# Kernel tuning notes

Hardware: AMD Instinct MI355X
Metric: run time of the kernel (lower is better)

The kernel has to match this reference:

```python
import jax, jax.numpy as jnp
import numpy as np

B, S, D, H = 4, 2048, 1024, 16
HD = D // H  # 64


def setup_inputs() -> dict:
    key = jax.random.key(0)
    ks = jax.random.split(key, 5)
    s = 1.0 / np.sqrt(D)
    return {
        "x": jax.random.normal(ks[0], (B, S, D), dtype=jnp.float32),
        "W_attn": jax.random.normal(ks[1], (D, 3 * D), dtype=jnp.float32) * s,
        "b_attn": jnp.zeros((3 * D,), dtype=jnp.float32),
        "W_proj": jax.random.normal(ks[2], (D, D), dtype=jnp.float32) * s,
        "b_proj": jnp.zeros((D,), dtype=jnp.float32),
    }


def reference(x, W_attn, b_attn, W_proj, b_proj):
    Bx, Sx, Dx = x.shape
    qkv = x @ W_attn + b_attn                      # [B,S,3D]
    q, k, v = jnp.split(qkv, 3, axis=-1)
    q = q.reshape(Bx, Sx, H, HD).transpose(0, 2, 1, 3)  # [B,H,S,hd]
    k = k.reshape(Bx, Sx, H, HD).transpose(0, 2, 1, 3)
    v = v.reshape(Bx, Sx, H, HD).transpose(0, 2, 1, 3)
    att = jnp.einsum('bhqd,bhkd->bhqk', q, k) * (HD ** -0.5)
    causal = jnp.tril(jnp.ones((Sx, Sx), dtype=bool))
    att = jnp.where(causal[None, None], att, -jnp.inf)
    att = jax.nn.softmax(att, axis=-1)
    y = jnp.einsum('bhqk,bhkd->bhqd', att, v)      # [B,H,S,hd]
    y = y.transpose(0, 2, 1, 3).reshape(Bx, Sx, Dx)
    return y @ W_proj + b_proj
```

## Files before the change

kernel.cpp:

```cpp
#include <hip/hip_runtime.h>
#include <hip/hip_bf16.h>
#include <math.h>


typedef __bf16 bf16;
typedef __bf16 bf16x8 __attribute__((ext_vector_type(8)));
typedef __bf16 bf16x4 __attribute__((ext_vector_type(4)));
typedef float f32x4 __attribute__((ext_vector_type(4)));

#define B_ 4
#define S_ 2048
#define D_ 1024
#define H_ 16
#define HD_ 64
#define QSCALE 0.1803368801f

#if __has_builtin(__builtin_amdgcn_exp2f)
#define EXP2F(x) __builtin_amdgcn_exp2f(x)
#else
#define EXP2F(x) exp2f(x)
#endif
#if __has_builtin(__builtin_amdgcn_rcpf)
#define RCPF(x) __builtin_amdgcn_rcpf(x)
#else
#define RCPF(x) (1.0f / (x))
#endif

#define GLOAD_LDS16(gptr, lptr)                                              \
    __builtin_amdgcn_global_load_lds(                                        \
        (const __attribute__((address_space(1))) void*)(uintptr_t)(gptr),    \
        (__attribute__((address_space(3))) void*)(uintptr_t)(lptr), 16, 0, 0)

__global__ void k_cvt(const float* __restrict__ in, bf16* __restrict__ out, int n) {
    int i = (blockIdx.x * 256 + threadIdx.x) * 4;
    if (i >= n) return;
    float4 v = *reinterpret_cast<const float4*>(in + i);
    bf16x4 o;
    o.x = (bf16)v.x; o.y = (bf16)v.y; o.z = (bf16)v.z; o.w = (bf16)v.w;
    *reinterpret_cast<bf16x4*>(out + i) = o;
}

__global__ void k_transpose_cvt(const float* __restrict__ W, bf16* __restrict__ WT,
                                int K, int N) {
    __shared__ float t[32][33];
    int n0 = blockIdx.x * 32, k0 = blockIdx.y * 32;
    int tx = threadIdx.x & 31, ty = threadIdx.x >> 5;
#pragma unroll
    for (int j = 0; j < 32; j += 8)
        t[ty + j][tx] = W[(size_t)(k0 + ty + j) * N + n0 + tx];
    __syncthreads();
#pragma unroll
    for (int j = 0; j < 32; j += 8)
        WT[(size_t)(n0 + ty + j) * K + k0 + tx] = (bf16)t[tx][ty + j];
}

template <int MODE>
__global__ __launch_bounds__(256) void k_gemm(
    const bf16* __restrict__ A, const bf16* __restrict__ BT,
    const float* __restrict__ bias,
    void* out0, void* out1, void* out2, int M, int N, int K) {
    __shared__ __align__(16) bf16 Asm[2][128][64];
    __shared__ __align__(16) bf16 Bsm[2][128][64];
    int mb = blockIdx.y * 128, nb = blockIdx.x * 128;
    int tid = threadIdx.x;
    int w = tid >> 6, lane = tid & 63, lo = lane & 15, qu = lane >> 4;
    int wm = (w >> 1) * 64, wn = (w & 1) * 64;
    int srow = lane >> 3, sch = lane & 7;
    int gch = (sch ^ srow) * 8;
    int r0 = w * 32;

    f32x4 zero = {0.f, 0.f, 0.f, 0.f};
    f32x4 acc[4][4];
#pragma unroll
    for (int i = 0; i < 4; i++)
#pragma unroll
        for (int j = 0; j < 4; j++) acc[i][j] = zero;

    const int nt = K >> 6;

    auto stage = [&](int t, int buf) {
        int kb = t * 64;
#pragma unroll
        for (int g = 0; g < 4; g++) {
            int row = r0 + g * 8;
            GLOAD_LDS16(A + (size_t)(mb + row + srow) * K + kb + gch,
                        &Asm[buf][row][0]);
            GLOAD_LDS16(BT + (size_t)(nb + row + srow) * K + kb + gch,
                        &Bsm[buf][row][0]);
        }
    };

    stage(0, 0);

    for (int t = 0; t < nt; t++) {
        int cur = t & 1;
        if (t + 1 < nt) {
            stage(t + 1, cur ^ 1);
            asm volatile("s_waitcnt vmcnt(8)" ::: "memory");
        } else {
            asm volatile("s_waitcnt vmcnt(0)" ::: "memory");
        }
        __builtin_amdgcn_s_barrier();
        asm volatile("" ::: "memory");
        bf16x8 af[4][2], bfr[4][2];
#pragma unroll
        for (int tt = 0; tt < 4; tt++)
#pragma unroll
            for (int ks = 0; ks < 2; ks++) {
                af[tt][ks] = *reinterpret_cast<const bf16x8*>(
                    &Asm[cur][wm + tt * 16 + lo][((ks * 4 + qu) ^ (lo & 7)) * 8]);
                bfr[tt][ks] = *reinterpret_cast<const bf16x8*>(
                    &Bsm[cur][wn + tt * 16 + lo][((ks * 4 + qu) ^ (lo & 7)) * 8]);
            }
        __builtin_amdgcn_s_setprio(1);
#pragma unroll
        for (int i = 0; i < 4; i++)
#pragma unroll
            for (int j = 0; j < 4; j++) {
                acc[i][j] = __builtin_amdgcn_mfma_f32_16x16x32_bf16(
                    af[i][0], bfr[j][0], acc[i][j], 0, 0, 0);
                acc[i][j] = __builtin_amdgcn_mfma_f32_16x16x32_bf16(
                    af[i][1], bfr[j][1], acc[i][j], 0, 0, 0);
            }
        __builtin_amdgcn_s_setprio(0);
        asm volatile("" ::: "memory");
        __builtin_amdgcn_s_barrier();
        asm volatile("" ::: "memory");
    }

#pragma unroll
    for (int i = 0; i < 4; i++) {
#pragma unroll
        for (int j = 0; j < 4; j++) {
            int col = nb + wn + j * 16 + lo;
            float bv = bias[col];
            float v4v[4];
#pragma unroll
            for (int r = 0; r < 4; r++) v4v[r] = acc[i][j][r] + bv;
            int row0 = mb + wm + i * 16 + qu * 4;
            if (MODE == 0) {
                int b = row0 >> 11, s0 = row0 & 2047;
                int which = col >> 10, rem = col & 1023;
                int h = rem >> 6, d = rem & 63;
                int bh = b * H_ + h;
                if (which == 2) {
                    bf16x4 pk;
#pragma unroll
                    for (int r = 0; r < 4; r++) pk[r] = (bf16)v4v[r];
                    *reinterpret_cast<bf16x4*>(
                        (bf16*)out2 + ((size_t)bh * HD_ + d) * S_ + s0) = pk;
                } else {
                    bf16* dst = which == 0 ? (bf16*)out0 : (bf16*)out1;
                    float sc = which == 0 ? QSCALE : 1.0f;
#pragma unroll
                    for (int r = 0; r < 4; r++)
                        dst[((size_t)bh * S_ + s0 + r) * HD_ + d] = (bf16)(v4v[r] * sc);
                }
            } else {
#pragma unroll
                for (int r = 0; r < 4; r++)
                    ((float*)out0)[(size_t)(row0 + r) * N + col] = v4v[r];
            }
        }
    }
}

__global__ __launch_bounds__(256) void k_attn(
    const bf16* __restrict__ Q, const bf16* __restrict__ K,
    const bf16* __restrict__ Vt, bf16* __restrict__ Y) {
    __shared__ __align__(16) bf16 Ks[2][64][64];
    __shared__ __align__(16) bf16 Vs[2][64][64];
    __shared__ __align__(16) bf16 Psm[4][32][68];
    int blk = blockIdx.x;
    int bh = blk & 63;
    int p = blk >> 6;
    int tid = threadIdx.x, w = tid >> 6, lane = tid & 63;
    int lo = lane & 15, qu = lane >> 4;
    int b = bh >> 4, h = bh & 15;
    const bf16* Qb = Q + (size_t)bh * S_ * HD_;
    const bf16* Kb = K + (size_t)bh * S_ * HD_;
    const bf16* Vb = Vt + (size_t)bh * HD_ * S_;

    bf16x8 onesf;
#pragma unroll
    for (int j = 0; j < 8; j++) onesf[j] = (bf16)1.0f;

    f32x4 zero = {0.f, 0.f, 0.f, 0.f};

    int r0 = w * 16;
    int lrow = lane >> 3, lch = lane & 7;
    int gch = (lch ^ lrow) * 8;

    auto stageKV = [&](int t, int buf) {
        int kb = t * 64;
#pragma unroll
        for (int s = 0; s < 2; s++) {
            int row = r0 + s * 8;
            GLOAD_LDS16(Kb + (size_t)(kb + row + lrow) * HD_ + gch,
                        &Ks[buf][row][0]);
            GLOAD_LDS16(Vb + (size_t)(row + lrow) * S_ + kb + gch,
                        &Vs[buf][row][0]);
        }
    };

    for (int half = 0; half < 2; half++) {
        int jb = half == 0 ? 15 - p : p;
        int qbase = jb * 128 + w * 32;
        int nt = 2 * jb + 2;

        bf16x8 qf[2][2];
#pragma unroll
        for (int i = 0; i < 2; i++)
#pragma unroll
            for (int ks = 0; ks < 2; ks++)
                qf[i][ks] = *reinterpret_cast<const bf16x8*>(
                    Qb + (size_t)(qbase + i * 16 + lo) * HD_ + ks * 32 + qu * 8);

        f32x4 o[2][4];
        f32x4 lacc[2];
#pragma unroll
        for (int i = 0; i < 2; i++) {
            lacc[i] = zero;
#pragma unroll
            for (int r = 0; r < 4; r++) o[i][r] = zero;
        }

        stageKV(0, 0);

        for (int t = 0; t < nt; t++) {
            int cur = t & 1;
            if (t + 1 < nt) {
                stageKV(t + 1, cur ^ 1);
                asm volatile("s_waitcnt vmcnt(8)" ::: "memory");
            } else {
                asm volatile("s_waitcnt vmcnt(0)" ::: "memory");
            }
            __builtin_amdgcn_s_barrier();
            asm volatile("" ::: "memory");
            int kb = t * 64;
            if (kb <= qbase + 31) {
                bf16x8 kf[4][2];
#pragma unroll
                for (int kc = 0; kc < 4; kc++)
#pragma unroll
                    for (int ks = 0; ks < 2; ks++)
                        kf[kc][ks] = *reinterpret_cast<const bf16x8*>(
                            &Ks[cur][kc * 16 + lo][((ks * 4 + qu) ^ (lo & 7)) * 8]);
                f32x4 sc[2][4];
                __builtin_amdgcn_s_setprio(1);
#pragma unroll
                for (int kc = 0; kc < 4; kc++)
#pragma unroll
                    for (int i = 0; i < 2; i++) {
                        f32x4 a = __builtin_amdgcn_mfma_f32_16x16x32_bf16(
                            qf[i][0], kf[kc][0], zero, 0, 0, 0);
                        sc[i][kc] = __builtin_amdgcn_mfma_f32_16x16x32_bf16(
                            qf[i][1], kf[kc][1], a, 0, 0, 0);
                    }
                __builtin_amdgcn_s_setprio(0);
                bf16x8 vfr[4][2];
#pragma unroll
                for (int nc = 0; nc < 4; nc++)
#pragma unroll
                    for (int ks = 0; ks < 2; ks++)
                        vfr[nc][ks] = *reinterpret_cast<const bf16x8*>(
                            &Vs[cur][nc * 16 + lo][((ks * 4 + qu) ^ (lo & 7)) * 8]);
                if (kb + 63 > qbase) {
#pragma unroll
                    for (int kc = 0; kc < 4; kc++) {
                        int kj = kb + kc * 16 + lo;
#pragma unroll
                        for (int i = 0; i < 2; i++) {
                            int qi = qbase + i * 16 + qu * 4;
#pragma unroll
                            for (int r = 0; r < 4; r++)
                                sc[i][kc][r] = (kj > qi + r) ? -1e30f : sc[i][kc][r];
                        }
                    }
                }
#pragma unroll
                for (int i = 0; i < 2; i++)
#pragma unroll
                    for (int kc = 0; kc < 4; kc++)
#pragma unroll
                        for (int r = 0; r < 4; r++)
                            sc[i][kc][r] = EXP2F(sc[i][kc][r]);
#pragma unroll
                for (int i = 0; i < 2; i++)
#pragma unroll
                    for (int kc = 0; kc < 4; kc++)
#pragma unroll
                        for (int r = 0; r < 4; r++)
                            Psm[w][i * 16 + qu * 4 + r][kc * 16 + lo] =
                                (bf16)sc[i][kc][r];
                asm volatile("s_waitcnt lgkmcnt(0)" ::: "memory");
                bf16x8 pa[2][2];
#pragma unroll
                for (int i = 0; i < 2; i++)
#pragma unroll
                    for (int ks = 0; ks < 2; ks++)
                        pa[i][ks] = *reinterpret_cast<const bf16x8*>(
                            &Psm[w][i * 16 + lo][ks * 32 + qu * 8]);
                __builtin_amdgcn_s_setprio(1);
#pragma unroll
                for (int i = 0; i < 2; i++) {
                    lacc[i] = __builtin_amdgcn_mfma_f32_16x16x32_bf16(
                        pa[i][0], onesf, lacc[i], 0, 0, 0);
                    lacc[i] = __builtin_amdgcn_mfma_f32_16x16x32_bf16(
                        pa[i][1], onesf, lacc[i], 0, 0, 0);
                }
#pragma unroll
                for (int nc = 0; nc < 4; nc++)
#pragma unroll
                    for (int i = 0; i < 2; i++) {
                        o[i][nc] = __builtin_amdgcn_mfma_f32_16x16x32_bf16(
                            pa[i][0], vfr[nc][0], o[i][nc], 0, 0, 0);
                        o[i][nc] = __builtin_amdgcn_mfma_f32_16x16x32_bf16(
                            pa[i][1], vfr[nc][1], o[i][nc], 0, 0, 0);
                    }
                __builtin_amdgcn_s_setprio(0);
            }
            asm volatile("" ::: "memory");
            __builtin_amdgcn_s_barrier();
            asm volatile("" ::: "memory");
        }

#pragma unroll
        for (int i = 0; i < 2; i++) {
#pragma unroll
            for (int r = 0; r < 4; r++) {
                float inv = RCPF(lacc[i][r]);
                int s = qbase + i * 16 + qu * 4 + r;
#pragma unroll
                for (int nc = 0; nc < 4; nc++) {
                    float v = o[i][nc][r] * inv;
                    Y[((size_t)(b * S_ + s) * H_ + h) * HD_ + nc * 16 + lo] = (bf16)v;
                }
            }
        }
    }
}

extern "C" void kernel_launch(void* const* d_in, const int* in_sizes, int n_in,
                              void* d_out, int out_size, void* d_ws, size_t ws_size,
                              hipStream_t stream) {
    const float* x      = (const float*)d_in[0];
    const float* W_attn = (const float*)d_in[1];
    const float* b_attn = (const float*)d_in[2];
    const float* W_proj = (const float*)d_in[3];
    const float* b_proj = (const float*)d_in[4];
    float* out = (float*)d_out;

    char* ws = (char*)d_ws;
    size_t off = 0;
    auto alloc = [&](size_t bytes) -> void* {
        void* p = ws + off;
        off += (bytes + 255) & ~(size_t)255;
        return p;
    };
    const size_t MD = (size_t)B_ * S_ * D_;
    bf16* xb  = (bf16*)alloc(MD * 2);
    bf16* wta = (bf16*)alloc((size_t)3 * D_ * D_ * 2);
    bf16* wtp = (bf16*)alloc((size_t)D_ * D_ * 2);
    bf16* Qb  = (bf16*)alloc(MD * 2);
    bf16* Kb  = (bf16*)alloc(MD * 2);
    bf16* Vtb = (bf16*)alloc(MD * 2);
    bf16* Ya  = (bf16*)alloc(MD * 2);

    k_cvt<<<8192, 256, 0, stream>>>(x, xb, (int)MD);
    k_transpose_cvt<<<dim3(96, 32), 256, 0, stream>>>(W_attn, wta, D_, 3 * D_);
    k_transpose_cvt<<<dim3(32, 32), 256, 0, stream>>>(W_proj, wtp, D_, D_);
    k_gemm<0><<<dim3(24, 64), 256, 0, stream>>>(xb, wta, b_attn, Qb, Kb, Vtb,
                                                B_ * S_, 3 * D_, D_);
    k_attn<<<dim3(512), 256, 0, stream>>>(Qb, Kb, Vtb, Ya);
    k_gemm<1><<<dim3(8, 64), 256, 0, stream>>>(Ya, wtp, b_proj, out, nullptr, nullptr,
                                               B_ * S_, D_, D_);
}
```

Measured before the change: 248.6 us.

## Run both causal query bands concurrently in 8-wave attention blocks sharing K/V tiles

The attention kernel now launches 512-thread blocks where waves 0-3 handle the heavy query band and waves 4-7 the light band at the same time, sharing the staged K/V tiles instead of processing the two bands sequentially. Block-to-band mapping is permuted for load balance. The score MFMA computes the transposed tile (K as A operand) so probabilities can be written to LDS as packed bf16x4 vectors rather than scalar stores. This halves K/V reloads for the light band and removes the sequential outer loop. The cost is that the light-band waves idle through most iterations, and the larger blocks raise register pressure.

```diff
diff --git a/kernel.cpp b/kernel.cpp
--- a/kernel.cpp
+++ b/kernel.cpp
@@ -165,177 +165,170 @@
     }
 }
 
-__global__ __launch_bounds__(256) void k_attn(
+__global__ __launch_bounds__(512, 4) void k_attn(
     const bf16* __restrict__ Q, const bf16* __restrict__ K,
     const bf16* __restrict__ Vt, bf16* __restrict__ Y) {
     __shared__ __align__(16) bf16 Ks[2][64][64];
     __shared__ __align__(16) bf16 Vs[2][64][64];
-    __shared__ __align__(16) bf16 Psm[4][32][68];
+    __shared__ __align__(16) bf16 Psm[8][32][68];
     int blk = blockIdx.x;
     int bh = blk & 63;
-    int p = blk >> 6;
+    int praw = blk >> 6;
+    int p = praw < 4 ? praw : 11 - praw;
     int tid = threadIdx.x, w = tid >> 6, lane = tid & 63;
     int lo = lane & 15, qu = lane >> 4;
     int b = bh >> 4, h = bh & 15;
+    int band = (w < 4) ? (15 - p) : p;
+    int qbase = band * 128 + (w & 3) * 32;
+    int nt = 32 - 2 * p;
     const bf16* Qb = Q + (size_t)bh * S_ * HD_;
     const bf16* Kb = K + (size_t)bh * S_ * HD_;
     const bf16* Vb = Vt + (size_t)bh * HD_ * S_;
 
+    bf16x8 qf[2][2];
+#pragma unroll
+    for (int i = 0; i < 2; i++)
+#pragma unroll
+        for (int ks = 0; ks < 2; ks++)
+            qf[i][ks] = *reinterpret_cast<const bf16x8*>(
+                Qb + (size_t)(qbase + i * 16 + lo) * HD_ + ks * 32 + qu * 8);
+
     bf16x8 onesf;
 #pragma unroll
     for (int j = 0; j < 8; j++) onesf[j] = (bf16)1.0f;
 
     f32x4 zero = {0.f, 0.f, 0.f, 0.f};
-
-    int r0 = w * 16;
+    f32x4 o[2][4];
+    f32x4 lacc[2];
+#pragma unroll
+    for (int i = 0; i < 2; i++) {
+        lacc[i] = zero;
+#pragma unroll
+        for (int r = 0; r < 4; r++) o[i][r] = zero;
+    }
+
+    int r0 = w * 8;
     int lrow = lane >> 3, lch = lane & 7;
     int gch = (lch ^ lrow) * 8;
 
     auto stageKV = [&](int t, int buf) {
         int kb = t * 64;
-#pragma unroll
-        for (int s = 0; s < 2; s++) {
-            int row = r0 + s * 8;
-            GLOAD_LDS16(Kb + (size_t)(kb + row + lrow) * HD_ + gch,
-                        &Ks[buf][row][0]);
-            GLOAD_LDS16(Vb + (size_t)(row + lrow) * S_ + kb + gch,
-                        &Vs[buf][row][0]);
-        }
+        GLOAD_LDS16(Kb + (size_t)(kb + r0 + lrow) * HD_ + gch, &Ks[buf][r0][0]);
+        GLOAD_LDS16(Vb + (size_t)(r0 + lrow) * S_ + kb + gch, &Vs[buf][r0][0]);
     };
 
-    for (int half = 0; half < 2; half++) {
-        int jb = half == 0 ? 15 - p : p;
-        int qbase = jb * 128 + w * 32;
-        int nt = 2 * jb + 2;
-
-        bf16x8 qf[2][2];
-#pragma unroll
-        for (int i = 0; i < 2; i++)
-#pragma unroll
-            for (int ks = 0; ks < 2; ks++)
-                qf[i][ks] = *reinterpret_cast<const bf16x8*>(
-                    Qb + (size_t)(qbase + i * 16 + lo) * HD_ + ks * 32 + qu * 8);
-
-        f32x4 o[2][4];
-        f32x4 lacc[2];
-#pragma unroll
-        for (int i = 0; i < 2; i++) {
-            lacc[i] = zero;
-#pragma unroll
-            for (int r = 0; r < 4; r++) o[i][r] = zero;
-        }
-
-        stageKV(0, 0);
-
-        for (int t = 0; t < nt; t++) {
-            int cur = t & 1;
-            if (t + 1 < nt) {
-                stageKV(t + 1, cur ^ 1);
-                asm volatile("s_waitcnt vmcnt(8)" ::: "memory");
-            } else {
-                asm volatile("s_waitcnt vmcnt(0)" ::: "memory");
-            }
-            __builtin_amdgcn_s_barrier();
-            asm volatile("" ::: "memory");
-            int kb = t * 64;
-            if (kb <= qbase + 31) {
-                bf16x8 kf[4][2];
-#pragma unroll
-                for (int kc = 0; kc < 4; kc++)
-#pragma unroll
-                    for (int ks = 0; ks < 2; ks++)
-                        kf[kc][ks] = *reinterpret_cast<const bf16x8*>(
-                            &Ks[cur][kc * 16 + lo][((ks * 4 + qu) ^ (lo & 7)) * 8]);
-                f32x4 sc[2][4];
-                __builtin_amdgcn_s_setprio(1);
-#pragma unroll
-                for (int kc = 0; kc < 4; kc++)
+    stageKV(0, 0);
+
+    for (int t = 0; t < nt; t++) {
+        int cur = t & 1;
+        if (t + 1 < nt) {
+            stageKV(t + 1, cur ^ 1);
+            asm volatile("s_waitcnt vmcnt(2)" ::: "memory");
+        } else {
+            asm volatile("s_waitcnt vmcnt(0)" ::: "memory");
+        }
+        __builtin_amdgcn_s_barrier();
+        asm volatile("" ::: "memory");
+        int kb = t * 64;
+        if (kb <= qbase + 31) {
+            bf16x8 kf[4][2];
+#pragma unroll
+            for (int kc = 0; kc < 4; kc++)
+#pragma unroll
+                for (int ks = 0; ks < 2; ks++)
+                    kf[kc][ks] = *reinterpret_cast<const bf16x8*>(
+                        &Ks[cur][kc * 16 + lo][((ks * 4 + qu) ^ (lo & 7)) * 8]);
+            f32x4 st[4][2];
+            __builtin_amdgcn_s_setprio(1);
+#pragma unroll
+            for (int kc = 0; kc < 4; kc++)
+#pragma unroll
+                for (int i = 0; i < 2; i++) {
+                    f32x4 a = __builtin_amdgcn_mfma_f32_16x16x32_bf16(
+                        kf[kc][0], qf[i][0], zero, 0, 0, 0);
+                    st[kc][i] = __builtin_amdgcn_mfma_f32_16x16x32_bf16(
+                        kf[kc][1], qf[i][1], a, 0, 0, 0);
+                }
+            __builtin_amdgcn_s_setprio(0);
+            if (kb + 63 > qbase) {
+#pragma unroll
+                for (int kc = 0; kc < 4; kc++) {
+                    int key = kb + kc * 16 + qu * 4;
 #pragma unroll
                     for (int i = 0; i < 2; i++) {
-                        f32x4 a = __builtin_amdgcn_mfma_f32_16x16x32_bf16(
-                            qf[i][0], kf[kc][0], zero, 0, 0, 0);
-                        sc[i][kc] = __builtin_amdgcn_mfma_f32_16x16x32_bf16(
-                            qf[i][1], kf[kc][1], a, 0, 0, 0);
+                        int q = qbase + i * 16 + lo;
+#pragma unroll
+                        for (int r = 0; r < 4; r++)
+                            st[kc][i][r] = (key + r > q) ? -1e30f : st[kc][i][r];
                     }
-                __builtin_amdgcn_s_setprio(0);
-                bf16x8 vfr[4][2];
-#pragma unroll
-                for (int nc = 0; nc < 4; nc++)
-#pragma unroll
-                    for (int ks = 0; ks < 2; ks++)
-                        vfr[nc][ks] = *reinterpret_cast<const bf16x8*>(
-                            &Vs[cur][nc * 16 + lo][((ks * 4 + qu) ^ (lo & 7)) * 8]);
-                if (kb + 63 > qbase) {
-#pragma unroll
-                    for (int kc = 0; kc < 4; kc++) {
-                        int kj = kb + kc * 16 + lo;
-#pragma unroll
-                        for (int i = 0; i < 2; i++) {
-                            int qi = qbase + i * 16 + qu * 4;
-#pragma unroll
-                            for (int r = 0; r < 4; r++)
-                                sc[i][kc][r] = (kj > qi + r) ? -1e30f : sc[i][kc][r];
-                        }
-                    }
-                }
+                }
+            }
+#pragma unroll
+            for (int kc = 0; kc < 4; kc++)
 #pragma unroll
                 for (int i = 0; i < 2; i++)
 #pragma unroll
-                    for (int kc = 0; kc < 4; kc++)
-#pragma unroll
-                        for (int r = 0; r < 4; r++)
-                            sc[i][kc][r] = EXP2F(sc[i][kc][r]);
-#pragma unroll
-                for (int i = 0; i < 2; i++)
-#pragma unroll
-                    for (int kc = 0; kc < 4; kc++)
-#pragma unroll
-                        for (int r = 0; r < 4; r++)
-                            Psm[w][i * 16 + qu * 4 + r][kc * 16 + lo] =
-                                (bf16)sc[i][kc][r];
-                asm volatile("s_waitcnt lgkmcnt(0)" ::: "memory");
-                bf16x8 pa[2][2];
-#pragma unroll
-                for (int i = 0; i < 2; i++)
-#pragma unroll
-                    for (int ks = 0; ks < 2; ks++)
-                        pa[i][ks] = *reinterpret_cast<const bf16x8*>(
-                            &Psm[w][i * 16 + lo][ks * 32 + qu * 8]);
-                __builtin_amdgcn_s_setprio(1);
+                    for (int r = 0; r < 4; r++)
+                        st[kc][i][r] = EXP2F(st[kc][i][r]);
+#pragma unroll
+            for (int i = 0; i < 2; i++)
+#pragma unroll
+                for (int kc = 0; kc < 4; kc++) {
+                    bf16x4 pk;
+#pragma unroll
+                    for (int r = 0; r < 4; r++) pk[r] = (bf16)st[kc][i][r];
+                    *reinterpret_cast<bf16x4*>(
+                        &Psm[w][i * 16 + lo][kc * 16 + qu * 4]) = pk;
+                }
+            asm volatile("s_waitcnt lgkmcnt(0)" ::: "memory");
+            bf16x8 pa[2][2];
+#pragma unroll
+            for (int i = 0; i < 2; i++)
+#pragma unroll
+                for (int ks = 0; ks < 2; ks++)
+                    pa[i][ks] = *reinterpret_cast<const bf16x8*>(
+                        &Psm[w][i * 16 + lo][ks * 32 + qu * 8]);
+            bf16x8 vfr[4][2];
+#pragma unroll
+            for (int nc = 0; nc < 4; nc++)
+#pragma unroll
+                for (int ks = 0; ks < 2; ks++)
+                    vfr[nc][ks] = *reinterpret_cast<const bf16x8*>(
+                        &Vs[cur][nc * 16 + lo][((ks * 4 + qu) ^ (lo & 7)) * 8]);
+            __builtin_amdgcn_s_setprio(1);
+#pragma unroll
+            for (int i = 0; i < 2; i++) {
+                lacc[i] = __builtin_amdgcn_mfma_f32_16x16x32_bf16(
+                    pa[i][0], onesf, lacc[i], 0, 0, 0);
+                lacc[i] = __builtin_amdgcn_mfma_f32_16x16x32_bf16(
+                    pa[i][1], onesf, lacc[i], 0, 0, 0);
+            }
+#pragma unroll
+            for (int nc = 0; nc < 4; nc++)
 #pragma unroll
                 for (int i = 0; i < 2; i++) {
-                    lacc[i] = __builtin_amdgcn_mfma_f32_16x16x32_bf16(
-                        pa[i][0], onesf, lacc[i], 0, 0, 0);
-                    lacc[i] = __builtin_amdgcn_mfma_f32_16x16x32_bf16(
-                        pa[i][1], onesf, lacc[i], 0, 0, 0);
-                }
-#pragma unroll
-                for (int nc = 0; nc < 4; nc++)
-#pragma unroll
-                    for (int i = 0; i < 2; i++) {
-                        o[i][nc] = __builtin_amdgcn_mfma_f32_16x16x32_bf16(
-                            pa[i][0], vfr[nc][0], o[i][nc], 0, 0, 0);
-                        o[i][nc] = __builtin_amdgcn_mfma_f32_16x16x32_bf16(
-                            pa[i][1], vfr[nc][1], o[i][nc], 0, 0, 0);
-                    }
-                __builtin_amdgcn_s_setprio(0);
-            }
-            asm volatile("" ::: "memory");
-            __builtin_amdgcn_s_barrier();
-            asm volatile("" ::: "memory");
-        }
-
-#pragma unroll
-        for (int i = 0; i < 2; i++) {
-#pragma unroll
-            for (int r = 0; r < 4; r++) {
-                float inv = RCPF(lacc[i][r]);
-                int s = qbase + i * 16 + qu * 4 + r;
-#pragma unroll
-                for (int nc = 0; nc < 4; nc++) {
-                    float v = o[i][nc][r] * inv;
-                    Y[((size_t)(b * S_ + s) * H_ + h) * HD_ + nc * 16 + lo] = (bf16)v;
-                }
+                    o[i][nc] = __builtin_amdgcn_mfma_f32_16x16x32_bf16(
+                        pa[i][0], vfr[nc][0], o[i][nc], 0, 0, 0);
+                    o[i][nc] = __builtin_amdgcn_mfma_f32_16x16x32_bf16(
+                        pa[i][1], vfr[nc][1], o[i][nc], 0, 0, 0);
+                }
+            __builtin_amdgcn_s_setprio(0);
+        }
+        asm volatile("" ::: "memory");
+        __builtin_amdgcn_s_barrier();
+        asm volatile("" ::: "memory");
+    }
+
+#pragma unroll
+    for (int i = 0; i < 2; i++) {
+#pragma unroll
+        for (int r = 0; r < 4; r++) {
+            float inv = RCPF(lacc[i][r]);
+            int s = qbase + i * 16 + qu * 4 + r;
+#pragma unroll
+            for (int nc = 0; nc < 4; nc++) {
+                float v = o[i][nc][r] * inv;
+                Y[((size_t)(b * S_ + s) * H_ + h) * HD_ + nc * 16 + lo] = (bf16)v;
             }
         }
     }
@@ -372,7 +365,7 @@
     k_transpose_cvt<<<dim3(32, 32), 256, 0, stream>>>(W_proj, wtp, D_, D_);
     k_gemm<0><<<dim3(24, 64), 256, 0, stream>>>(xb, wta, b_attn, Qb, Kb, Vtb,
                                                 B_ * S_, 3 * D_, D_);
-    k_attn<<<dim3(512), 256, 0, stream>>>(Qb, Kb, Vtb, Ya);
+    k_attn<<<dim3(512), 512, 0, stream>>>(Qb, Kb, Vtb, Ya);
     k_gemm<1><<<dim3(8, 64), 256, 0, stream>>>(Ya, wtp, b_proj, out, nullptr, nullptr,
                                                B_ * S_, D_, D_);
 }
```

Result: faster. 236.4 us (-4.9%).
